# Optimization experiments

Hardware: AMD Instinct MI355X
Metric: run time of the kernel (lower is better)

The kernel has to match this reference:

```python
import jax, jax.numpy as jnp
import numpy as np

K = 5           # kernel_size from kernel_kwargs
P = K // 2      # padding (same-size output)
MASK_TH = 0.5   # mask_th init kwarg
EPS = 1e-6

# squared distance of each of the K*K taps from the kernel center, shape [K*K]
_R2 = jnp.asarray(np.array([(dy - P) ** 2 + (dx - P) ** 2
                            for dy in range(K) for dx in range(K)], dtype=np.float32))


def setup_inputs() -> dict:
    key = jax.random.key(0)
    k1, k2 = jax.random.split(key)
    bev_map = jax.random.normal(k1, (4, 1, 768, 768), dtype=jnp.float32)
    # per-pixel scales in [0.5, 2.0) -- realistic kernel bandwidths
    bev_scale = 0.5 + 1.5 * jax.random.uniform(k2, (4, 1, 768, 768), dtype=jnp.float32)
    return {"bev_map": bev_map, "bev_scale": bev_scale}


def reference(bev_map, bev_scale):
    B, C, H, W = bev_map.shape
    x = jax.nn.relu(bev_map)                                   # non_neg = ReLU
    xp = jnp.pad(x, ((0, 0), (0, 0), (P, P), (P, P)))
    # unfold: [B, C, K*K, H, W] shifted views of the padded map
    patches = jnp.stack([xp[:, :, dy:dy + H, dx:dx + W]
                         for dy in range(K) for dx in range(K)], axis=2)
    # ScaleAdaptiveExpKernel: Gaussian weights from per-pixel scale
    # w: [B, 1, K*K, H, W]
    w = jnp.exp(-_R2[None, None, :, None, None]
                / (2.0 * jnp.square(bev_scale)[:, :, None] + EPS))
    bev_map_conv = jnp.sum(patches * w, axis=2)                # [B, C, H, W]
    mask = (bev_map_conv >= MASK_TH).astype(bev_map_conv.dtype)
    return bev_map_conv, mask
```

## Files before the change

kernel.cpp:

```cpp
#include <hip/hip_runtime.h>

#define HH 768
#define WW 768
#define BC 4
#define NPIX (BC * HH * WW)

typedef float f4 __attribute__((ext_vector_type(4)));
typedef float f2 __attribute__((ext_vector_type(2)));

__global__ __launch_bounds__(512) void conv_thresh_kernel(
    const float* __restrict__ bev_map,
    const float* __restrict__ bev_scale,
    float* __restrict__ out)
{
    const int tx = threadIdx.x;
    const int ty = threadIdx.y;
    const int x0 = (blockIdx.x * 64 + tx) * 4;
    const int y0 = blockIdx.y * 16 + ty * 2;
    const int b  = blockIdx.z;

    const size_t plane = (size_t)b * (HH * WW);
    const float* __restrict__ m = bev_map + plane;

    const bool leftok  = (x0 != 0);
    const bool rightok = (x0 != WW - 4);

    float h0[6][4], h1[6][4], h2[6][4];

#pragma unroll
    for (int r = 0; r < 6; ++r) {
        const int yy = y0 - 2 + r;
        const bool yok = (unsigned)yy < (unsigned)HH;
        const float* rowp = m + yy * WW + x0;
        float w[8];
        if (yok) {
            f4 t = *(const f4*)rowp;
            w[2] = fmaxf(t.x, 0.f); w[3] = fmaxf(t.y, 0.f);
            w[4] = fmaxf(t.z, 0.f); w[5] = fmaxf(t.w, 0.f);
            if (leftok) {
                f2 t2 = *(const f2*)(rowp - 2);
                w[0] = fmaxf(t2.x, 0.f); w[1] = fmaxf(t2.y, 0.f);
            } else { w[0] = 0.f; w[1] = 0.f; }
            if (rightok) {
                f2 t2 = *(const f2*)(rowp + 4);
                w[6] = fmaxf(t2.x, 0.f); w[7] = fmaxf(t2.y, 0.f);
            } else { w[6] = 0.f; w[7] = 0.f; }
        } else {
#pragma unroll
            for (int i = 0; i < 8; ++i) w[i] = 0.f;
        }
#pragma unroll
        for (int j = 0; j < 4; ++j) {
            h0[r][j] = w[j + 2];
            h1[r][j] = w[j + 1] + w[j + 3];
            h2[r][j] = w[j]     + w[j + 4];
        }
    }

#pragma unroll
    for (int k = 0; k < 2; ++k) {
        const int oy = y0 + k;
        const size_t idx = plane + (size_t)oy * WW + x0;
        const f4 scv = __builtin_nontemporal_load((const f4*)(bev_scale + idx));
        f4 conv, mask;
#pragma unroll
        for (int j = 0; j < 4; ++j) {
            const float c0 = h0[k + 2][j];
            const float s1 = h1[k + 2][j] + h0[k + 1][j] + h0[k + 3][j];
            const float s2 = h1[k + 1][j] + h1[k + 3][j];
            const float s4 = h2[k + 2][j] + h0[k][j]     + h0[k + 4][j];
            const float s5 = h2[k + 1][j] + h2[k + 3][j] + h1[k][j] + h1[k + 4][j];
            const float s8 = h2[k][j]     + h2[k + 4][j];

            const float sc = scv[j];
            const float t1 = -1.0f / (2.0f * sc * sc + 1e-6f);
            const float e1 = __expf(t1);
            const float e2 = e1 * e1;
            const float e4 = e2 * e2;
            const float e5 = e4 * e1;
            const float e8 = e4 * e4;

            float cv = c0;
            cv = fmaf(e1, s1, cv);
            cv = fmaf(e2, s2, cv);
            cv = fmaf(e4, s4, cv);
            cv = fmaf(e5, s5, cv);
            cv = fmaf(e8, s8, cv);
            conv[j] = cv;
            mask[j] = (cv >= 0.5f) ? 1.0f : 0.0f;
        }
        __builtin_nontemporal_store(conv, (f4*)(out + idx));
        __builtin_nontemporal_store(mask, (f4*)(out + idx + (size_t)NPIX));
    }
}

extern "C" void kernel_launch(void* const* d_in, const int* in_sizes, int n_in,
                              void* d_out, int out_size, void* d_ws, size_t ws_size,
                              hipStream_t stream) {
    const float* bev_map   = (const float*)d_in[0];
    const float* bev_scale = (const float*)d_in[1];
    float* out = (float*)d_out;

    dim3 block(64, 8, 1);
    dim3 grid(WW / 256, HH / 16, BC);
    conv_thresh_kernel<<<grid, block, 0, stream>>>(bev_map, bev_scale, out);
}
```

Baseline: 83.40 us.

## Share horizontal halo via wave shuffles, shrink blocks, drop nontemporal hints

```diff
diff --git a/kernel.cpp b/kernel.cpp
--- a/kernel.cpp
+++ b/kernel.cpp
@@ -8,7 +8,7 @@
 typedef float f4 __attribute__((ext_vector_type(4)));
 typedef float f2 __attribute__((ext_vector_type(2)));
 
-__global__ __launch_bounds__(512) void conv_thresh_kernel(
+__global__ __launch_bounds__(256) void conv_thresh_kernel(
     const float* __restrict__ bev_map,
     const float* __restrict__ bev_scale,
     float* __restrict__ out)
@@ -16,14 +16,11 @@
     const int tx = threadIdx.x;
     const int ty = threadIdx.y;
     const int x0 = (blockIdx.x * 64 + tx) * 4;
-    const int y0 = blockIdx.y * 16 + ty * 2;
+    const int y0 = blockIdx.y * 8 + ty * 2;
     const int b  = blockIdx.z;
 
     const size_t plane = (size_t)b * (HH * WW);
     const float* __restrict__ m = bev_map + plane;
-
-    const bool leftok  = (x0 != 0);
-    const bool rightok = (x0 != WW - 4);
 
     float h0[6][4], h1[6][4], h2[6][4];
 
@@ -32,36 +29,45 @@
         const int yy = y0 - 2 + r;
         const bool yok = (unsigned)yy < (unsigned)HH;
         const float* rowp = m + yy * WW + x0;
-        float w[8];
+        f4 t;
         if (yok) {
-            f4 t = *(const f4*)rowp;
-            w[2] = fmaxf(t.x, 0.f); w[3] = fmaxf(t.y, 0.f);
-            w[4] = fmaxf(t.z, 0.f); w[5] = fmaxf(t.w, 0.f);
-            if (leftok) {
+            t = *(const f4*)rowp;
+            t.x = fmaxf(t.x, 0.f); t.y = fmaxf(t.y, 0.f);
+            t.z = fmaxf(t.z, 0.f); t.w = fmaxf(t.w, 0.f);
+        } else {
+            t.x = 0.f; t.y = 0.f; t.z = 0.f; t.w = 0.f;
+        }
+        float lz = __shfl_up(t.z, 1);
+        float lw = __shfl_up(t.w, 1);
+        float rx = __shfl_down(t.x, 1);
+        float ry = __shfl_down(t.y, 1);
+        if (tx == 0) {
+            lz = 0.f; lw = 0.f;
+            if (yok && x0 != 0) {
                 f2 t2 = *(const f2*)(rowp - 2);
-                w[0] = fmaxf(t2.x, 0.f); w[1] = fmaxf(t2.y, 0.f);
-            } else { w[0] = 0.f; w[1] = 0.f; }
-            if (rightok) {
+                lz = fmaxf(t2.x, 0.f); lw = fmaxf(t2.y, 0.f);
+            }
+        }
+        if (tx == 63) {
+            rx = 0.f; ry = 0.f;
+            if (yok && x0 != WW - 4) {
                 f2 t2 = *(const f2*)(rowp + 4);
-                w[6] = fmaxf(t2.x, 0.f); w[7] = fmaxf(t2.y, 0.f);
-            } else { w[6] = 0.f; w[7] = 0.f; }
-        } else {
-#pragma unroll
-            for (int i = 0; i < 8; ++i) w[i] = 0.f;
+                rx = fmaxf(t2.x, 0.f); ry = fmaxf(t2.y, 0.f);
+            }
         }
-#pragma unroll
-        for (int j = 0; j < 4; ++j) {
-            h0[r][j] = w[j + 2];
-            h1[r][j] = w[j + 1] + w[j + 3];
-            h2[r][j] = w[j]     + w[j + 4];
-        }
+        const float w0 = lz, w1 = lw, w2 = t.x, w3 = t.y,
+                    w4 = t.z, w5 = t.w, w6 = rx, w7 = ry;
+        h0[r][0] = w2; h1[r][0] = w1 + w3; h2[r][0] = w0 + w4;
+        h0[r][1] = w3; h1[r][1] = w2 + w4; h2[r][1] = w1 + w5;
+        h0[r][2] = w4; h1[r][2] = w3 + w5; h2[r][2] = w2 + w6;
+        h0[r][3] = w5; h1[r][3] = w4 + w6; h2[r][3] = w3 + w7;
     }
 
 #pragma unroll
     for (int k = 0; k < 2; ++k) {
         const int oy = y0 + k;
         const size_t idx = plane + (size_t)oy * WW + x0;
-        const f4 scv = __builtin_nontemporal_load((const f4*)(bev_scale + idx));
+        const f4 scv = *(const f4*)(bev_scale + idx);
         f4 conv, mask;
 #pragma unroll
         for (int j = 0; j < 4; ++j) {
@@ -89,8 +95,8 @@
             conv[j] = cv;
             mask[j] = (cv >= 0.5f) ? 1.0f : 0.0f;
         }
-        __builtin_nontemporal_store(conv, (f4*)(out + idx));
-        __builtin_nontemporal_store(mask, (f4*)(out + idx + (size_t)NPIX));
+        *(f4*)(out + idx) = conv;
+        *(f4*)(out + idx + (size_t)NPIX) = mask;
     }
 }
 
@@ -101,7 +107,7 @@
     const float* bev_scale = (const float*)d_in[1];
     float* out = (float*)d_out;
 
-    dim3 block(64, 8, 1);
-    dim3 grid(WW / 256, HH / 16, BC);
+    dim3 block(64, 4, 1);
+    dim3 grid(WW / 256, HH / 8, BC);
     conv_thresh_kernel<<<grid, block, 0, stream>>>(bev_map, bev_scale, out);
 }
```

After: 76.44 us (median of 2 runs). -8.3%, faster.
